# Kernel tuning notes

Hardware: AMD Instinct MI355X
Metric: run time of the kernel (lower is better)

## Reference

```python
import jax, jax.numpy as jnp
import numpy as np

B, T_SRC, T_TGT, C_IN, C_OUT = 8, 4096, 2048, 1024, 1024
LN_EPS = 1e-5


def _prefix_mask(lens, T):
    return (jnp.arange(T)[None, :] < lens[:, None]).astype(jnp.int32)


def setup_inputs() -> dict:
    key = jax.random.key(0)
    ks = jax.random.split(key, 6)
    src = jax.random.normal(ks[0], (B, T_SRC, C_IN), dtype=jnp.float32)
    tgt = jax.random.normal(ks[1], (B, T_TGT, C_IN), dtype=jnp.float32)
    # ragged prefix lengths; first row full so src_sizes.max() == T_SRC (static result width)
    src_lens = jax.random.randint(ks[2], (B,), T_SRC // 2, T_SRC + 1).at[0].set(T_SRC)
    tgt_lens = jax.random.randint(ks[3], (B,), T_TGT // 2, T_TGT + 1).at[0].set(T_TGT)
    src_mask = _prefix_mask(src_lens, T_SRC)
    tgt_mask = _prefix_mask(tgt_lens, T_TGT)
    conv_w = jax.random.normal(ks[4], (C_OUT, C_IN), dtype=jnp.float32) * 0.02
    conv_b = jax.random.normal(ks[5], (C_OUT,), dtype=jnp.float32) * 0.02
    ln_g = jnp.ones((C_OUT,), dtype=jnp.float32)
    ln_b = jnp.zeros((C_OUT,), dtype=jnp.float32)
    return {"src": src, "src_mask": src_mask, "tgt": tgt, "tgt_mask": tgt_mask,
            "conv_w": conv_w, "conv_b": conv_b, "ln_g": ln_g, "ln_b": ln_b}


def reference(src, src_mask, tgt, tgt_mask, conv_w, conv_b, ln_g, ln_b):
    # kernel-size-1 Conv1d == per-token linear: [B,T_tgt,C_in] @ W^T + b
    y = jnp.einsum("btc,oc->bto", tgt, conv_w) + conv_b  # [B, T_tgt, C_out]

    src_sizes = src_mask.sum(-1).astype(jnp.int32)  # [B]
    tgt_sizes = tgt_mask.sum(-1).astype(jnp.int32)  # [B]

    # Batched nearest-neighbor ragged resize: out pos j maps to floor(j*tgt/src)
    j = jnp.arange(src.shape[1], dtype=jnp.int32)  # [T_src]
    safe_src = jnp.maximum(src_sizes, 1)[:, None]
    idx = (j[None, :] * tgt_sizes[:, None]) // safe_src  # [B, T_src]
    idx = jnp.clip(idx, 0, jnp.maximum(tgt_sizes, 1)[:, None] - 1)
    gathered = jnp.take_along_axis(y, idx[:, :, None], axis=1)  # [B, T_src, C_out]
    valid = (j[None, :] < src_sizes[:, None])[:, :, None]
    upsampled = jnp.where(valid, gathered, 0.0)

    # LayerNorm over channel dim (applied to all positions, incl. zero padding, as in torch)
    mu = upsampled.mean(-1, keepdims=True)
    var = jnp.mean(jnp.square(upsampled - mu), axis=-1, keepdims=True)
    out = (upsampled - mu) * jax.lax.rsqrt(var + LN_EPS) * ln_g + ln_b
    return (out, src_mask)
```

## Files before the change

kernel.cpp:

```cpp
#include <hip/hip_runtime.h>

#define NB   8
#define TSRC 4096
#define TTGT 2048
#define CH   1024
#define BK   64

typedef __attribute__((ext_vector_type(4))) float  f32x4;
typedef __attribute__((ext_vector_type(8))) __bf16 bf16x8;
typedef __attribute__((ext_vector_type(4))) __bf16 bf16x4;

__device__ __forceinline__ void async16(const void* g, void* l) {
  __builtin_amdgcn_global_load_lds((const __attribute__((address_space(1))) void*)g,
                                   (__attribute__((address_space(3))) void*)l, 16, 0, 0);
}

__global__ __launch_bounds__(256) void prep_kernel(const float* __restrict__ tgt,
                                                   const float* __restrict__ W,
                                                   const int* __restrict__ src_mask,
                                                   const int* __restrict__ tgt_mask,
                                                   __bf16* __restrict__ Abf,
                                                   __bf16* __restrict__ Wbf,
                                                   int* __restrict__ sizes,
                                                   float* __restrict__ mask_out) {
  const int bx = blockIdx.x;
  const int t  = threadIdx.x;
  const int NCONV = NB * TTGT + CH;
  if (bx < NCONV) {
    const float* sp;
    __bf16* dp;
    if (bx < NB * TTGT) { sp = tgt + (size_t)bx * CH; dp = Abf + (size_t)bx * CH; }
    else { const int r = bx - NB * TTGT; sp = W + (size_t)r * CH; dp = Wbf + (size_t)r * CH; }
    const float4 v = ((const float4*)sp)[t];
    bf16x4 u = {(__bf16)v.x, (__bf16)v.y, (__bf16)v.z, (__bf16)v.w};
    *(bf16x4*)(dp + t * 4) = u;
  } else if (bx < NCONV + 16) {
    const int id = bx - NCONV;
    const int b  = id & 7;
    const int* m = (id < 8) ? (src_mask + (size_t)b * TSRC) : (tgt_mask + (size_t)b * TTGT);
    const int T  = (id < 8) ? TSRC : TTGT;
    int s = 0;
    for (int i = t; i < T; i += 256) s += m[i];
#pragma unroll
    for (int off = 32; off > 0; off >>= 1) s += __shfl_down(s, off);
    __shared__ int red[4];
    if ((t & 63) == 0) red[t >> 6] = s;
    __syncthreads();
    if (t == 0) sizes[id] = red[0] + red[1] + red[2] + red[3];
  } else {
    const int i = (bx - (NCONV + 16)) * 256 + t;
    mask_out[i] = (float)src_mask[i];
  }
}

__global__ __launch_bounds__(512) void gemm_kernel(const __bf16* __restrict__ A,
                                                   const __bf16* __restrict__ Bw,
                                                   const float* __restrict__ bias,
                                                   const int* __restrict__ sizes,
                                                   __bf16* __restrict__ y) {
  const int bid = blockIdx.x;
  const int Mt  = bid & 63;
  const int Nt  = bid >> 6;
  const int n0 = Nt * 128;
  const int m0 = Mt * 256;
  const int b  = m0 >> 11;
  const int t0 = m0 & (TTGT - 1);
  if (t0 >= sizes[8 + b]) return;

  __shared__ __bf16 As[256 * BK];
  __shared__ __bf16 Bs[128 * BK];

  const int tid  = threadIdx.x;
  const int lane = tid & 63;
  const int wave = tid >> 6;
  const int wm   = (wave >> 1) * 64;
  const int wn   = (wave & 1) * 64;
  const int lr   = lane & 15;
  const int quad = lane >> 4;

  const int srow = tid >> 3;
  const int scol = (tid & 7) * 8;
  const __bf16* gA = A  + ((size_t)(m0 + srow)) * CH + scol;
  const __bf16* gB = Bw + ((size_t)(n0 + srow)) * CH + scol;
  __bf16* lA = As + tid * 8;
  __bf16* lB = Bs + tid * 8;

  f32x4 acc[4][4];
  const f32x4 z = {0.f, 0.f, 0.f, 0.f};
#pragma unroll
  for (int i = 0; i < 4; ++i)
#pragma unroll
    for (int j = 0; j < 4; ++j) acc[i][j] = z;

  for (int kb = 0; kb < CH; kb += BK) {
#pragma unroll
    for (int q = 0; q < 4; ++q)
      async16(gA + (size_t)q * 64 * CH + kb, lA + q * 4096);
#pragma unroll
    for (int q = 0; q < 2; ++q)
      async16(gB + (size_t)q * 64 * CH + kb, lB + q * 4096);
    __syncthreads();
#pragma unroll
    for (int ko = 0; ko < 2; ++ko) {
      bf16x8 af[4], bf[4];
#pragma unroll
      for (int i = 0; i < 4; ++i)
        af[i] = *(const bf16x8*)(As + (wm + i * 16 + lr) * BK + ko * 32 + quad * 8);
#pragma unroll
      for (int j = 0; j < 4; ++j)
        bf[j] = *(const bf16x8*)(Bs + (wn + j * 16 + lr) * BK + ko * 32 + quad * 8);
#pragma unroll
      for (int i = 0; i < 4; ++i)
#pragma unroll
        for (int j = 0; j < 4; ++j)
          acc[i][j] = __builtin_amdgcn_mfma_f32_16x16x32_bf16(af[i], bf[j], acc[i][j], 0, 0, 0);
    }
    __syncthreads();
  }

#pragma unroll
  for (int i = 0; i < 4; ++i) {
    const int mrow = m0 + wm + i * 16 + quad * 4;
#pragma unroll
    for (int j = 0; j < 4; ++j) {
      const int ncol = n0 + wn + j * 16 + lr;
      const float bv = bias[ncol];
      __bf16* yp = y + (size_t)mrow * CH + ncol;
#pragma unroll
      for (int r = 0; r < 4; ++r) yp[(size_t)r * CH] = (__bf16)(acc[i][j][r] + bv);
    }
  }
}

__global__ __launch_bounds__(256) void ln_kernel(const __bf16* __restrict__ y,
                                                 const int* __restrict__ sizes,
                                                 const float* __restrict__ g,
                                                 const float* __restrict__ be,
                                                 float* __restrict__ out) {
  const int wid = (blockIdx.x * 256 + threadIdx.x) >> 6;
  const int l   = threadIdx.x & 63;

  float gr[16], br[16];
#pragma unroll
  for (int h = 0; h < 2; ++h) {
    const int base = h * 512 + l * 8;
    *(f32x4*)(gr + h * 8)     = *(const f32x4*)(g + base);
    *(f32x4*)(gr + h * 8 + 4) = *(const f32x4*)(g + base + 4);
    *(f32x4*)(br + h * 8)     = *(const f32x4*)(be + base);
    *(f32x4*)(br + h * 8 + 4) = *(const f32x4*)(be + base + 4);
  }

#pragma unroll
  for (int rr = 0; rr < 4; ++rr) {
    const int row = wid + rr * 8192;
    const int b   = row >> 12;
    const int j   = row & (TSRC - 1);
    const int ss  = sizes[b];
    const int tg  = sizes[8 + b];
    float v[16];
    if (j < ss) {
      const int den = (ss > 0) ? ss : 1;
      int ii = (int)(((long long)j * (long long)tg) / den);
      const int hi = ((tg > 1) ? tg : 1) - 1;
      ii = (ii > hi) ? hi : ((ii < 0) ? 0 : ii);
      const __bf16* yr = y + ((size_t)b * TTGT + ii) * CH;
      const bf16x8 u0 = *(const bf16x8*)(yr + l * 8);
      const bf16x8 u1 = *(const bf16x8*)(yr + 512 + l * 8);
#pragma unroll
      for (int k = 0; k < 8; ++k) { v[k] = (float)u0[k]; v[8 + k] = (float)u1[k]; }
    } else {
#pragma unroll
      for (int k = 0; k < 16; ++k) v[k] = 0.f;
    }
    float s = 0.f, q = 0.f;
#pragma unroll
    for (int k = 0; k < 16; ++k) { s += v[k]; q += v[k] * v[k]; }
#pragma unroll
    for (int off = 32; off > 0; off >>= 1) {
      s += __shfl_xor(s, off);
      q += __shfl_xor(q, off);
    }
    const float mu = s * (1.0f / CH);
    float var = q * (1.0f / CH) - mu * mu;
    var = fmaxf(var, 0.0f);
    const float rs = rsqrtf(var + 1e-5f);
    float* orow = out + (size_t)row * CH;
#pragma unroll
    for (int h = 0; h < 2; ++h) {
      const int base = h * 512 + l * 8;
      f32x4 o0, o1;
      o0[0] = (v[h * 8 + 0] - mu) * rs * gr[h * 8 + 0] + br[h * 8 + 0];
      o0[1] = (v[h * 8 + 1] - mu) * rs * gr[h * 8 + 1] + br[h * 8 + 1];
      o0[2] = (v[h * 8 + 2] - mu) * rs * gr[h * 8 + 2] + br[h * 8 + 2];
      o0[3] = (v[h * 8 + 3] - mu) * rs * gr[h * 8 + 3] + br[h * 8 + 3];
      o1[0] = (v[h * 8 + 4] - mu) * rs * gr[h * 8 + 4] + br[h * 8 + 4];
      o1[1] = (v[h * 8 + 5] - mu) * rs * gr[h * 8 + 5] + br[h * 8 + 5];
      o1[2] = (v[h * 8 + 6] - mu) * rs * gr[h * 8 + 6] + br[h * 8 + 6];
      o1[3] = (v[h * 8 + 7] - mu) * rs * gr[h * 8 + 7] + br[h * 8 + 7];
      *(f32x4*)(orow + base)     = o0;
      *(f32x4*)(orow + base + 4) = o1;
    }
  }
}

__global__ __launch_bounds__(256) void fallback_kernel(const float* __restrict__ tgt,
                                                       const int* __restrict__ src_mask,
                                                       const int* __restrict__ tgt_mask,
                                                       const float* __restrict__ W,
                                                       const float* __restrict__ bias,
                                                       const float* __restrict__ g,
                                                       const float* __restrict__ be,
                                                       float* __restrict__ out,
                                                       float* __restrict__ mask_out) {
  const int bx = blockIdx.x;
  const int b  = bx >> 12;
  const int j  = bx & (TSRC - 1);
  const int t  = threadIdx.x;
  int s1 = 0, s2 = 0;
  for (int i = t; i < TSRC; i += 256) s1 += src_mask[(size_t)b * TSRC + i];
  for (int i = t; i < TTGT; i += 256) s2 += tgt_mask[(size_t)b * TTGT + i];
#pragma unroll
  for (int off = 32; off > 0; off >>= 1) { s1 += __shfl_down(s1, off); s2 += __shfl_down(s2, off); }
  __shared__ int ired[8];
  if ((t & 63) == 0) { ired[t >> 6] = s1; ired[4 + (t >> 6)] = s2; }
  __syncthreads();
  const int ss = ired[0] + ired[1] + ired[2] + ired[3];
  const int tg = ired[4] + ired[5] + ired[6] + ired[7];
  const bool valid = j < ss;
  int ii = 0;
  if (valid) {
    const int den = (ss > 0) ? ss : 1;
    ii = (int)(((long long)j * (long long)tg) / den);
    const int hi = ((tg > 1) ? tg : 1) - 1;
    if (ii > hi) ii = hi;
    if (ii < 0) ii = 0;
  }
  __shared__ float trow[CH];
  const float* tr = tgt + ((size_t)b * TTGT + ii) * CH;
  for (int i = t; i < CH; i += 256) trow[i] = valid ? tr[i] : 0.0f;
  __syncthreads();
  float4 v = make_float4(0.f, 0.f, 0.f, 0.f);
  if (valid) {
    float a0 = 0.f, a1 = 0.f, a2 = 0.f, a3 = 0.f;
    const float* w0 = W + (size_t)(4 * t + 0) * CH;
    const float* w1 = W + (size_t)(4 * t + 1) * CH;
    const float* w2 = W + (size_t)(4 * t + 2) * CH;
    const float* w3 = W + (size_t)(4 * t + 3) * CH;
    for (int k = 0; k < CH; ++k) {
      const float x = trow[k];
      a0 += x * w0[k]; a1 += x * w1[k]; a2 += x * w2[k]; a3 += x * w3[k];
    }
    v.x = a0 + bias[4 * t + 0];
    v.y = a1 + bias[4 * t + 1];
    v.z = a2 + bias[4 * t + 2];
    v.w = a3 + bias[4 * t + 3];
  }
  float s  = v.x + v.y + v.z + v.w;
  float sq = v.x * v.x + v.y * v.y + v.z * v.z + v.w * v.w;
#pragma unroll
  for (int off = 32; off > 0; off >>= 1) {
    s  += __shfl_down(s, off);
    sq += __shfl_down(sq, off);
  }
  __shared__ float red[8];
  __shared__ float stats[2];
  if ((t & 63) == 0) { red[t >> 6] = s; red[4 + (t >> 6)] = sq; }
  __syncthreads();
  if (t == 0) {
    const float S  = red[0] + red[1] + red[2] + red[3];
    const float Q  = red[4] + red[5] + red[6] + red[7];
    const float mu = S * (1.0f / CH);
    float var = Q * (1.0f / CH) - mu * mu;
    var = fmaxf(var, 0.0f);
    stats[0] = mu;
    stats[1] = rsqrtf(var + 1e-5f);
  }
  __syncthreads();
  const float mu = stats[0], rs = stats[1];
  const float4 gg = ((const float4*)g)[t];
  const float4 bb = ((const float4*)be)[t];
  float4 o;
  o.x = (v.x - mu) * rs * gg.x + bb.x;
  o.y = (v.y - mu) * rs * gg.y + bb.y;
  o.z = (v.z - mu) * rs * gg.z + bb.z;
  o.w = (v.w - mu) * rs * gg.w + bb.w;
  ((float4*)(out + ((size_t)b * TSRC + j) * CH))[t] = o;
  if (t == 0) mask_out[bx] = (float)src_mask[bx];
}

extern "C" void kernel_launch(void* const* d_in, const int* in_sizes, int n_in,
                              void* d_out, int out_size, void* d_ws, size_t ws_size,
                              hipStream_t stream) {
  (void)in_sizes; (void)n_in; (void)out_size;
  const int*   src_mask = (const int*)d_in[1];
  const float* tgt      = (const float*)d_in[2];
  const int*   tgt_mask = (const int*)d_in[3];
  const float* conv_w   = (const float*)d_in[4];
  const float* conv_b   = (const float*)d_in[5];
  const float* ln_g     = (const float*)d_in[6];
  const float* ln_b     = (const float*)d_in[7];

  float* out      = (float*)d_out;
  float* mask_out = out + (size_t)NB * TSRC * CH;

  const size_t M       = (size_t)NB * TTGT;
  const size_t off_abf = 256;
  const size_t off_wbf = off_abf + M * CH * 2;
  const size_t off_y   = off_wbf + (size_t)CH * CH * 2;
  const size_t need    = off_y + M * CH * 2;

  if (ws_size >= need) {
    int*    sizes = (int*)d_ws;
    __bf16* Abf   = (__bf16*)((char*)d_ws + off_abf);
    __bf16* Wbf   = (__bf16*)((char*)d_ws + off_wbf);
    __bf16* y     = (__bf16*)((char*)d_ws + off_y);
    prep_kernel<<<NB * TTGT + CH + 16 + 128, 256, 0, stream>>>(tgt, conv_w, src_mask, tgt_mask,
                                                               Abf, Wbf, sizes, mask_out);
    gemm_kernel<<<512, 512, 0, stream>>>(Abf, Wbf, conv_b, sizes, y);
    ln_kernel<<<2048, 256, 0, stream>>>(y, sizes, ln_g, ln_b, out);
  } else {
    fallback_kernel<<<NB * TSRC, 256, 0, stream>>>(tgt, src_mask, tgt_mask, conv_w, conv_b,
                                                   ln_g, ln_b, out, mask_out);
  }
}
```

Baseline: 306.3 us.

## Double-buffer GEMM LDS tiles with K-step 32 to overlap loads and MFMA

The GEMM main loop now uses two LDS buffers with a K-step of 32 instead of a single 64-wide buffer. The async global-to-LDS loads for the next K slice are issued before the MFMA work on the current slice, with one barrier per iteration. The goal is to hide global load latency behind compute instead of stalling at a barrier before each tile. The trade-off is twice as many loop iterations with smaller tiles, and LDS row strides that may cause bank conflicts.

```diff
diff --git a/kernel.cpp b/kernel.cpp
--- a/kernel.cpp
+++ b/kernel.cpp
@@ -4,7 +4,6 @@
 #define TSRC 4096
 #define TTGT 2048
 #define CH   1024
-#define BK   64
 
 typedef __attribute__((ext_vector_type(4))) float  f32x4;
 typedef __attribute__((ext_vector_type(8))) __bf16 bf16x8;
@@ -67,8 +66,8 @@
   const int t0 = m0 & (TTGT - 1);
   if (t0 >= sizes[8 + b]) return;
 
-  __shared__ __bf16 As[256 * BK];
-  __shared__ __bf16 Bs[128 * BK];
+  __shared__ __bf16 As[2 * 256 * 32];
+  __shared__ __bf16 Bs[2 * 128 * 32];
 
   const int tid  = threadIdx.x;
   const int lane = tid & 63;
@@ -78,8 +77,8 @@
   const int lr   = lane & 15;
   const int quad = lane >> 4;
 
-  const int srow = tid >> 3;
-  const int scol = (tid & 7) * 8;
+  const int srow = tid >> 2;
+  const int scol = (tid & 3) * 8;
   const __bf16* gA = A  + ((size_t)(m0 + srow)) * CH + scol;
   const __bf16* gB = Bw + ((size_t)(n0 + srow)) * CH + scol;
   __bf16* lA = As + tid * 8;
@@ -92,29 +91,35 @@
 #pragma unroll
     for (int j = 0; j < 4; ++j) acc[i][j] = z;
 
-  for (int kb = 0; kb < CH; kb += BK) {
-#pragma unroll
-    for (int q = 0; q < 4; ++q)
-      async16(gA + (size_t)q * 64 * CH + kb, lA + q * 4096);
-#pragma unroll
-    for (int q = 0; q < 2; ++q)
-      async16(gB + (size_t)q * 64 * CH + kb, lB + q * 4096);
-    __syncthreads();
-#pragma unroll
-    for (int ko = 0; ko < 2; ++ko) {
-      bf16x8 af[4], bf[4];
-#pragma unroll
-      for (int i = 0; i < 4; ++i)
-        af[i] = *(const bf16x8*)(As + (wm + i * 16 + lr) * BK + ko * 32 + quad * 8);
+  async16(gA, lA);
+  async16(gA + (size_t)128 * CH, lA + 4096);
+  async16(gB, lB);
+  __syncthreads();
+
+  const int NIT = CH / 32;
+  for (int it = 0; it < NIT; ++it) {
+    const int cur = it & 1;
+    if (it + 1 < NIT) {
+      const int nxt = cur ^ 1;
+      const int kb  = (it + 1) * 32;
+      async16(gA + kb, lA + nxt * 8192);
+      async16(gA + (size_t)128 * CH + kb, lA + nxt * 8192 + 4096);
+      async16(gB + kb, lB + nxt * 4096);
+    }
+    const __bf16* Ab = As + cur * 8192;
+    const __bf16* Bb = Bs + cur * 4096;
+    bf16x8 af[4], bf[4];
+#pragma unroll
+    for (int i = 0; i < 4; ++i)
+      af[i] = *(const bf16x8*)(Ab + (wm + i * 16 + lr) * 32 + quad * 8);
+#pragma unroll
+    for (int j = 0; j < 4; ++j)
+      bf[j] = *(const bf16x8*)(Bb + (wn + j * 16 + lr) * 32 + quad * 8);
+#pragma unroll
+    for (int i = 0; i < 4; ++i)
 #pragma unroll
       for (int j = 0; j < 4; ++j)
-        bf[j] = *(const bf16x8*)(Bs + (wn + j * 16 + lr) * BK + ko * 32 + quad * 8);
-#pragma unroll
-      for (int i = 0; i < 4; ++i)
-#pragma unroll
-        for (int j = 0; j < 4; ++j)
-          acc[i][j] = __builtin_amdgcn_mfma_f32_16x16x32_bf16(af[i], bf[j], acc[i][j], 0, 0, 0);
-    }
+        acc[i][j] = __builtin_amdgcn_mfma_f32_16x16x32_bf16(af[i], bf[j], acc[i][j], 0, 0, 0);
     __syncthreads();
   }
 
```

After: 302.6 us. About the same (-1.2%).
